# Performance work log

Hardware: AMD Instinct MI355X
Metric: run time of the kernel (lower is better)

Reference implementation:

```python
import jax, jax.numpy as jnp
import numpy as np

NEG = -1e30  # finite stand-in for -inf so logaddexp grads stay NaN-free


def setup_inputs() -> dict:
    key = jax.random.key(0)
    k1, k2 = jax.random.split(key)
    B, T, V, L = 32, 1024, 1024, 100
    logits = jax.random.normal(k1, (B, T, V), dtype=jnp.float32)
    # labels exclude the blank symbol (blank = V-1)
    targets = jax.random.randint(k2, (B, L), 0, V - 1, dtype=jnp.int32)
    return {"targets": targets, "logits": logits}


def reference(targets, logits):
    # tf.nn.ctc_loss(targets, logits, L, T, logits_time_major=False, blank_index=-1)
    # followed by reduce_mean. Standard CTC forward algorithm in log space.
    B, T, V = logits.shape
    L = targets.shape[1]
    S = 2 * L + 1
    blank = V - 1

    logp = jax.nn.log_softmax(logits, axis=-1)  # [B,T,V]

    # extended label sequence: blank, l1, blank, l2, ..., blank  -> [B,S]
    ext = jnp.full((B, S), blank, dtype=targets.dtype).at[:, 1::2].set(targets)
    # skip transition s-2 -> s allowed iff ext[s] != blank and ext[s] != ext[s-2]
    allow_skip = jnp.pad((ext[:, 2:] != blank) & (ext[:, 2:] != ext[:, :-2]),
                         ((0, 0), (2, 0)))  # [B,S]

    # gather per-step log-probs of extended labels: [B,T,S] -> [T,B,S]
    lp_ext = jnp.take_along_axis(logp, ext[:, None, :], axis=2)
    lp_ext = jnp.transpose(lp_ext, (1, 0, 2))

    alpha0 = (jnp.full((B, S), NEG, dtype=logp.dtype)
              .at[:, 0].set(lp_ext[0, :, 0])
              .at[:, 1].set(lp_ext[0, :, 1]))

    def step(alpha, lp_t):
        a1 = jnp.pad(alpha[:, :-1], ((0, 0), (1, 0)), constant_values=NEG)
        a2 = jnp.where(allow_skip,
                       jnp.pad(alpha[:, :-2], ((0, 0), (2, 0)), constant_values=NEG),
                       NEG)
        alpha_new = jnp.logaddexp(jnp.logaddexp(alpha, a1), a2) + lp_t
        return alpha_new, None

    alphaT, _ = jax.lax.scan(step, alpha0, lp_ext[1:])
    per_example_loss = -jnp.logaddexp(alphaT[:, -1], alphaT[:, -2])  # [B]
    return jnp.mean(per_example_loss)
```

## Files before the change

### kernel.cpp

```cpp
#include <hip/hip_runtime.h>
#include <math.h>

#define DEV static __device__ __forceinline__

constexpr int Bn = 32, Tn = 1024, Vn = 1024, Ln = 100, Sn = 2 * Ln + 1;
constexpr float LN2F = 0.6931471805599453f;
constexpr int   TILE = 32;

typedef const __attribute__((address_space(1))) unsigned int* as1_u32p;
typedef __attribute__((address_space(3))) unsigned int*       as3_u32p;

DEV void async16(const float* g, float* l) {
    __builtin_amdgcn_global_load_lds((as1_u32p)g, (as3_u32p)l, 16, 0, 0);
}
#define WAITVM32() asm volatile("s_waitcnt vmcnt(32)" ::: "memory")
#define WAITVM0()  asm volatile("s_waitcnt vmcnt(0)"  ::: "memory")

DEV float dpp_up1_f(float v) {
    return __builtin_bit_cast(float,
        __builtin_amdgcn_update_dpp(0, __builtin_bit_cast(int, v), 0x138, 0xf, 0xf, false));
}
DEV int dpp_up1_i(int v) {
    return __builtin_amdgcn_update_dpp(v, v, 0x138, 0xf, 0xf, false);
}

DEV float wave_max(float m) {
    #pragma unroll
    for (int off = 32; off; off >>= 1) m = fmaxf(m, __shfl_xor(m, off));
    return m;
}
DEV float wave_sum(float s) {
    #pragma unroll
    for (int off = 32; off; off >>= 1) s += __shfl_xor(s, off);
    return s;
}

__global__ __launch_bounds__(256) void pre_kernel(const int* __restrict__ targets,
                                                  const float* __restrict__ logits,
                                                  float* __restrict__ lp_ext) {
    __shared__ float rows[2][Vn];
    __shared__ float red[2][8];
    const int t    = threadIdx.x;
    const int lane = t & 63;
    const int wid  = t >> 6;
    const int r0   = blockIdx.x * 2;
    const int b    = r0 >> 10;

    float4 v0 = ((const float4*)(logits + (size_t)r0 * Vn))[t];
    float4 v1 = ((const float4*)(logits + (size_t)(r0 + 1) * Vn))[t];
    ((float4*)rows[0])[t] = v0;
    ((float4*)rows[1])[t] = v1;

    float m0 = fmaxf(fmaxf(v0.x, v0.y), fmaxf(v0.z, v0.w));
    float m1 = fmaxf(fmaxf(v1.x, v1.y), fmaxf(v1.z, v1.w));
    m0 = wave_max(m0); m1 = wave_max(m1);
    if (lane == 0) { red[0][wid] = m0; red[1][wid] = m1; }
    __syncthreads();
    m0 = fmaxf(fmaxf(red[0][0], red[0][1]), fmaxf(red[0][2], red[0][3]));
    m1 = fmaxf(fmaxf(red[1][0], red[1][1]), fmaxf(red[1][2], red[1][3]));

    float e0 = __expf(v0.x - m0) + __expf(v0.y - m0) + __expf(v0.z - m0) + __expf(v0.w - m0);
    float e1 = __expf(v1.x - m1) + __expf(v1.y - m1) + __expf(v1.z - m1) + __expf(v1.w - m1);
    e0 = wave_sum(e0); e1 = wave_sum(e1);
    if (lane == 0) { red[0][4 + wid] = e0; red[1][4 + wid] = e1; }
    __syncthreads();
    const float lse0 = m0 + __logf((red[0][4] + red[0][5]) + (red[0][6] + red[0][7]));
    const float lse1 = m1 + __logf((red[1][4] + red[1][5]) + (red[1][6] + red[1][7]));

    int ei = ((t & 1) && t < Sn) ? targets[b * Ln + (t >> 1)] : (Vn - 1);
    lp_ext[(size_t)r0 * 256 + t]       = __expf(rows[0][ei] - lse0);
    lp_ext[(size_t)(r0 + 1) * 256 + t] = __expf(rows[1][ei] - lse1);
}

__global__ __launch_bounds__(64, 1) void ctc_kernel(const int* __restrict__ targets,
                                                    const float* __restrict__ lp_ext,
                                                    float* __restrict__ loss) {
    __shared__ float tile[2][TILE * 256];
    const int b    = blockIdx.x;
    const int lane = threadIdx.x;

    float sk1f = 0.f, sk3f = 0.f;
    {
        const int* tg = targets + b * Ln;
        int s1 = 4 * lane + 1, s3 = 4 * lane + 3;
        if (s1 >= 3 && s1 < Sn) sk1f = (tg[s1 >> 1] != tg[(s1 - 3) >> 1]) ? 1.f : 0.f;
        if (s3 >= 3 && s3 < Sn) sk3f = (tg[s3 >> 1] != tg[(s3 - 3) >> 1]) ? 1.f : 0.f;
    }
    WAITVM0();

    const float* gb = lp_ext + (size_t)b * Tn * 256;
    #pragma unroll
    for (int u = 0; u < TILE; u++)
        async16(gb + (size_t)u * 256 + lane * 4, &tile[0][u * 256]);
    #pragma unroll
    for (int u = 0; u < TILE; u++)
        async16(gb + (size_t)(TILE + u) * 256 + lane * 4, &tile[1][u * 256]);

    float m0 = (lane == 0) ? 1.0f : 0.0f, m1 = 0.f, m2 = 0.f, m3 = 0.f;
    int   E  = 0;
    int   dE = 0;

    const int nt = Tn / TILE;

    auto consume_tile = [&](const float* cur) {
        float4 pr[TILE];
        #pragma unroll
        for (int u = 0; u < TILE; u++)
            pr[u] = ((const float4*)(cur + u * 256))[lane];
        #pragma unroll
        for (int u = 0; u < TILE; u++) {
            const float4 p = pr[u];
            float pmm = dpp_up1_f(m3);
            float pm1 = __builtin_amdgcn_ldexpf(pmm, dE);
            float n0 = (m0 + pm1) * p.x;
            float n1 = fmaf(pm1, sk1f, m0 + m1) * p.y;
            float n2 = (m2 + m1) * p.z;
            float n3 = fmaf(m1, sk3f, m2 + m3) * p.w;
            m0 = n0; m1 = n1; m2 = n2; m3 = n3;
            if ((u & 3) == 3) {
                float mx = fmaxf(fmaxf(m0, m1), fmaxf(m2, m3));
                int k = __builtin_amdgcn_frexp_expf(mx);
                int Enb_old = dpp_up1_i(E);
                E = (mx > 0.f) ? (E + k) : Enb_old;
                m0 = __builtin_amdgcn_ldexpf(m0, -k);
                m1 = __builtin_amdgcn_ldexpf(m1, -k);
                m2 = __builtin_amdgcn_ldexpf(m2, -k);
                m3 = __builtin_amdgcn_ldexpf(m3, -k);
                dE = dpp_up1_i(E) - E;
            }
        }
    };

    for (int tb = 0; tb < nt - 1; tb++) {
        WAITVM32();
        const float* cur = tile[tb & 1];
        consume_tile(cur);
        if (tb + 2 < nt) {
            float* nxt = tile[tb & 1];
            const float* gn = gb + (size_t)(tb + 2) * TILE * 256;
            #pragma unroll
            for (int u = 0; u < TILE; u++)
                async16(gn + (size_t)u * 256 + lane * 4, &nxt[u * 256]);
        }
    }
    WAITVM0();
    consume_tile(tile[(nt - 1) & 1]);

    float q200 = __shfl(m0, 50); int E50 = __shfl(E, 50);
    float q199 = __shfl(m3, 49); int E49 = __shfl(E, 49);
    if (lane == 0) {
        float s = q200 + __builtin_amdgcn_ldexpf(q199, E49 - E50);
        loss[b] = -LN2F * ((float)E50 + __log2f(s));
    }
}

__global__ __launch_bounds__(64) void mean_kernel(const float* __restrict__ loss,
                                                  float* __restrict__ out) {
    int lane = threadIdx.x;
    float v = (lane < Bn) ? loss[lane] : 0.f;
    #pragma unroll
    for (int off = 32; off; off >>= 1) v += __shfl_xor(v, off);
    if (lane == 0) out[0] = v * (1.0f / Bn);
}

extern "C" void kernel_launch(void* const* d_in, const int* in_sizes, int n_in,
                              void* d_out, int out_size, void* d_ws, size_t ws_size,
                              hipStream_t stream) {
    const int*   targets = (const int*)d_in[0];
    const float* logits  = (const float*)d_in[1];

    float* lp_ext = (float*)d_ws;
    float* loss   = (float*)((char*)d_ws + (size_t)Bn * Tn * 256 * sizeof(float) + 4096);

    pre_kernel<<<Bn * Tn / 2, 256, 0, stream>>>(targets, logits, lp_ext);
    ctc_kernel<<<Bn, 64, 0, stream>>>(targets, lp_ext, loss);
    mean_kernel<<<1, 64, 0, stream>>>(loss, (float*)d_out);
}
```

Baseline: 242.7 us.

## Shrink lp_ext row stride to 208 and prefetch directly into registers

Cuts the intermediate per-step label probability row from 256 to 208 floats, so only the 201 useful entries plus padding are written and read. The CTC recurrence kernel drops the LDS double buffer with async global-to-LDS loads and instead double-buffers two 32-step register arrays filled by plain global float4 loads. Lanes past 52 clamp to the last valid column. This reduces memory traffic and removes LDS round-trips, but relies on the compiler scheduling the register loads to overlap with compute and raises register pressure.

```diff
diff --git a/kernel.cpp b/kernel.cpp
--- a/kernel.cpp
+++ b/kernel.cpp
@@ -4,17 +4,9 @@
 #define DEV static __device__ __forceinline__
 
 constexpr int Bn = 32, Tn = 1024, Vn = 1024, Ln = 100, Sn = 2 * Ln + 1;
+constexpr int   RW   = 208;
 constexpr float LN2F = 0.6931471805599453f;
 constexpr int   TILE = 32;
-
-typedef const __attribute__((address_space(1))) unsigned int* as1_u32p;
-typedef __attribute__((address_space(3))) unsigned int*       as3_u32p;
-
-DEV void async16(const float* g, float* l) {
-    __builtin_amdgcn_global_load_lds((as1_u32p)g, (as3_u32p)l, 16, 0, 0);
-}
-#define WAITVM32() asm volatile("s_waitcnt vmcnt(32)" ::: "memory")
-#define WAITVM0()  asm volatile("s_waitcnt vmcnt(0)"  ::: "memory")
 
 DEV float dpp_up1_f(float v) {
     return __builtin_bit_cast(float,
@@ -67,15 +59,16 @@
     const float lse0 = m0 + __logf((red[0][4] + red[0][5]) + (red[0][6] + red[0][7]));
     const float lse1 = m1 + __logf((red[1][4] + red[1][5]) + (red[1][6] + red[1][7]));
 
-    int ei = ((t & 1) && t < Sn) ? targets[b * Ln + (t >> 1)] : (Vn - 1);
-    lp_ext[(size_t)r0 * 256 + t]       = __expf(rows[0][ei] - lse0);
-    lp_ext[(size_t)(r0 + 1) * 256 + t] = __expf(rows[1][ei] - lse1);
+    if (t < RW) {
+        int ei = ((t & 1) && t < Sn) ? targets[b * Ln + (t >> 1)] : (Vn - 1);
+        lp_ext[(size_t)r0 * RW + t]       = __expf(rows[0][ei] - lse0);
+        lp_ext[(size_t)(r0 + 1) * RW + t] = __expf(rows[1][ei] - lse1);
+    }
 }
 
 __global__ __launch_bounds__(64, 1) void ctc_kernel(const int* __restrict__ targets,
                                                     const float* __restrict__ lp_ext,
                                                     float* __restrict__ loss) {
-    __shared__ float tile[2][TILE * 256];
     const int b    = blockIdx.x;
     const int lane = threadIdx.x;
 
@@ -86,27 +79,21 @@
         if (s1 >= 3 && s1 < Sn) sk1f = (tg[s1 >> 1] != tg[(s1 - 3) >> 1]) ? 1.f : 0.f;
         if (s3 >= 3 && s3 < Sn) sk3f = (tg[s3 >> 1] != tg[(s3 - 3) >> 1]) ? 1.f : 0.f;
     }
-    WAITVM0();
 
-    const float* gb = lp_ext + (size_t)b * Tn * 256;
+    const float4* gb = (const float4*)(lp_ext + (size_t)b * Tn * RW);
+    const int ll = (lane < 52) ? lane : 51;
+
+    float4 bufA[TILE], bufB[TILE];
     #pragma unroll
-    for (int u = 0; u < TILE; u++)
-        async16(gb + (size_t)u * 256 + lane * 4, &tile[0][u * 256]);
+    for (int u = 0; u < TILE; u++) bufA[u] = gb[(size_t)u * 52 + ll];
     #pragma unroll
-    for (int u = 0; u < TILE; u++)
-        async16(gb + (size_t)(TILE + u) * 256 + lane * 4, &tile[1][u * 256]);
+    for (int u = 0; u < TILE; u++) bufB[u] = gb[(size_t)(TILE + u) * 52 + ll];
 
     float m0 = (lane == 0) ? 1.0f : 0.0f, m1 = 0.f, m2 = 0.f, m3 = 0.f;
     int   E  = 0;
     int   dE = 0;
 
-    const int nt = Tn / TILE;
-
-    auto consume_tile = [&](const float* cur) {
-        float4 pr[TILE];
-        #pragma unroll
-        for (int u = 0; u < TILE; u++)
-            pr[u] = ((const float4*)(cur + u * 256))[lane];
+    auto consume = [&](float4 (&pr)[TILE]) {
         #pragma unroll
         for (int u = 0; u < TILE; u++) {
             const float4 p = pr[u];
@@ -131,20 +118,21 @@
         }
     };
 
-    for (int tb = 0; tb < nt - 1; tb++) {
-        WAITVM32();
-        const float* cur = tile[tb & 1];
-        consume_tile(cur);
+    const int nt = Tn / TILE;
+    for (int tb = 0; tb < nt; tb += 2) {
+        consume(bufA);
         if (tb + 2 < nt) {
-            float* nxt = tile[tb & 1];
-            const float* gn = gb + (size_t)(tb + 2) * TILE * 256;
             #pragma unroll
             for (int u = 0; u < TILE; u++)
-                async16(gn + (size_t)u * 256 + lane * 4, &nxt[u * 256]);
+                bufA[u] = gb[(size_t)((tb + 2) * TILE + u) * 52 + ll];
+        }
+        consume(bufB);
+        if (tb + 3 < nt) {
+            #pragma unroll
+            for (int u = 0; u < TILE; u++)
+                bufB[u] = gb[(size_t)((tb + 3) * TILE + u) * 52 + ll];
         }
     }
-    WAITVM0();
-    consume_tile(tile[(nt - 1) & 1]);
 
     float q200 = __shfl(m0, 50); int E50 = __shfl(E, 50);
     float q199 = __shfl(m3, 49); int E49 = __shfl(E, 49);
@@ -170,7 +158,7 @@
     const float* logits  = (const float*)d_in[1];
 
     float* lp_ext = (float*)d_ws;
-    float* loss   = (float*)((char*)d_ws + (size_t)Bn * Tn * 256 * sizeof(float) + 4096);
+    float* loss   = (float*)((char*)d_ws + (size_t)Bn * Tn * RW * sizeof(float) + 4096);
 
     pre_kernel<<<Bn * Tn / 2, 256, 0, stream>>>(targets, logits, lp_ext);
     ctc_kernel<<<Bn, 64, 0, stream>>>(targets, lp_ext, loss);
```

Result: slower. 251.0 us (+3.4%).
